# Kernel optimization log

Measured on AMD Instinct MI355X. Metric: run time of the kernel, lower is better.

## Reference

```python
import jax, jax.numpy as jnp
import numpy as np

D_MODEL = 1024
NUM_HEADS = 16
D_K = D_MODEL // NUM_HEADS
B, T = 2, 2048


def setup_inputs() -> dict:
    key = jax.random.key(0)
    ks = jax.random.split(key, 9)
    s = 1.0 / np.sqrt(D_MODEL)
    inp = {"x": jax.random.normal(ks[0], (B, T, D_MODEL), dtype=jnp.float32)}
    for i, name in enumerate(["q", "k", "v", "out"]):
        inp[f"W_{name}"] = jax.random.uniform(ks[1 + 2 * i], (D_MODEL, D_MODEL), jnp.float32, -s, s)
        inp[f"b_{name}"] = jax.random.uniform(ks[2 + 2 * i], (D_MODEL,), jnp.float32, -s, s)
    return inp


def reference(x, W_q, b_q, W_k, b_k, W_v, b_v, W_out, b_out):
    b, t, _ = x.shape
    # torch Linear: y = x @ W.T + b
    def proj(inp, W, bias):
        y = inp @ W.T + bias
        return y.reshape(b, -1, NUM_HEADS, D_K).transpose(0, 2, 1, 3)  # [B,H,T,d_k]

    Q = proj(x, W_q, b_q)
    K = proj(x, W_k, b_k)
    V = proj(x, W_v, b_v)
    scores = jnp.einsum("bhqd,bhkd->bhqk", Q, K) / jnp.sqrt(jnp.float32(D_K))
    attn = jax.nn.softmax(scores, axis=-1)
    ctx = jnp.einsum("bhqk,bhkd->bhqd", attn, V)
    ctx = ctx.transpose(0, 2, 1, 3).reshape(b, t, D_MODEL)
    return ctx @ W_out.T + b_out
```

## Files before the change

kernel.cpp:

```cpp
#include <hip/hip_runtime.h>
#include <hip/hip_bf16.h>

typedef __attribute__((ext_vector_type(8))) short short8;
typedef __attribute__((ext_vector_type(4))) float floatx4;

__device__ __forceinline__ unsigned short f2b(float f) {
  unsigned int v;
  __builtin_memcpy(&v, &f, 4);
  unsigned int r = (v + 0x7FFFu + ((v >> 16) & 1u)) >> 16;
  return (unsigned short)r;
}

__device__ __forceinline__ unsigned int f2b_pk(float a, float b) {
#if __has_builtin(__builtin_amdgcn_cvt_pk_bf16_f32)
  typedef __attribute__((ext_vector_type(2))) __bf16 bf16x2;
  bf16x2 r = __builtin_amdgcn_cvt_pk_bf16_f32(a, b);
  unsigned int u;
  __builtin_memcpy(&u, &r, 4);
  return u;
#else
  return ((unsigned int)f2b(b) << 16) | (unsigned int)f2b(a);
#endif
}

__device__ __forceinline__ float fast_exp2(float x) {
#if __has_builtin(__builtin_amdgcn_exp2f)
  return __builtin_amdgcn_exp2f(x);
#else
  return __builtin_exp2f(x);
#endif
}

__device__ __forceinline__ void async_copy16(const void* g, void* l) {
  __builtin_amdgcn_global_load_lds(
      (const __attribute__((address_space(1))) unsigned int*)g,
      (__attribute__((address_space(3))) unsigned int*)l, 16, 0, 0);
}

#define QSCALE 0.18033688011112042f

__global__ __launch_bounds__(256) void cvt_all_kernel(
    const float* __restrict__ x,
    const float* __restrict__ w0, const float* __restrict__ w1,
    const float* __restrict__ w2, const float* __restrict__ w3,
    unsigned short* __restrict__ xb,
    unsigned short* __restrict__ d0, unsigned short* __restrict__ d1,
    unsigned short* __restrict__ d2, unsigned short* __restrict__ d3)
{
  int gid = blockIdx.x * 256 + threadIdx.x;
  const float* src;
  unsigned short* dst;
  size_t off;
  if (gid < (1 << 20)) {
    src = x; dst = xb; off = gid;
  } else {
    int g = gid - (1 << 20);
    int w = g >> 18;
    off = g & 0x3FFFF;
    src = (w == 0) ? w0 : (w == 1) ? w1 : (w == 2) ? w2 : w3;
    dst = (w == 0) ? d0 : (w == 1) ? d1 : (w == 2) ? d2 : d3;
  }
  floatx4 v = *(const floatx4*)(src + off * 4);
  unsigned int lo = f2b_pk(v[0], v[1]), hi = f2b_pk(v[2], v[3]);
  unsigned long long r = ((unsigned long long)hi << 32) | lo;
  *(unsigned long long*)(dst + off * 4) = r;
}

__global__ __launch_bounds__(256) void gemm_qkv_kernel(
    const unsigned short* __restrict__ A,
    const unsigned short* __restrict__ W0, const unsigned short* __restrict__ W1,
    const unsigned short* __restrict__ W2,
    const float* __restrict__ bias0, const float* __restrict__ bias1,
    const float* __restrict__ bias2,
    unsigned short* __restrict__ Qo, unsigned short* __restrict__ Ko,
    unsigned short* __restrict__ VTo)
{
  const int z = blockIdx.z;
  const unsigned short* W  = (z == 0) ? W0 : (z == 1) ? W1 : W2;
  const float* bias        = (z == 0) ? bias0 : (z == 1) ? bias1 : bias2;

  __shared__ alignas(16) unsigned short sA[128 * 32];
  __shared__ alignas(16) unsigned short sB[128 * 32];

  const int tid  = threadIdx.x;
  const int lane = tid & 63;
  const int wave = tid >> 6;
  const int col  = lane & 15;
  const int quad = lane >> 4;
  const int wm   = (wave >> 1) * 64;
  const int wn   = (wave & 1) * 64;
  const int m0   = blockIdx.y * 128;
  const int n0   = blockIdx.x * 128;

  floatx4 acc[4][4];
#pragma unroll
  for (int i = 0; i < 4; ++i)
#pragma unroll
    for (int j = 0; j < 4; ++j) acc[i][j] = (floatx4){0.f, 0.f, 0.f, 0.f};

  for (int k0 = 0; k0 < 1024; k0 += 32) {
    __syncthreads();
#pragma unroll
    for (int i = 0; i < 2; ++i) {
      int c   = i * 256 + tid;
      int row = c >> 2;
      int ko  = (c & 3) * 8;
      async_copy16(A + (size_t)(m0 + row) * 1024 + k0 + ko, sA + c * 8);
      async_copy16(W + (size_t)(n0 + row) * 1024 + k0 + ko, sB + c * 8);
    }
    __syncthreads();
    short8 af[4], bf[4];
#pragma unroll
    for (int mi = 0; mi < 4; ++mi)
      af[mi] = *(const short8*)(sA + (wm + mi * 16 + col) * 32 + quad * 8);
#pragma unroll
    for (int ni = 0; ni < 4; ++ni)
      bf[ni] = *(const short8*)(sB + (wn + ni * 16 + col) * 32 + quad * 8);
#pragma unroll
    for (int mi = 0; mi < 4; ++mi)
#pragma unroll
      for (int ni = 0; ni < 4; ++ni)
        acc[mi][ni] = __builtin_amdgcn_mfma_f32_16x16x32_bf16(af[mi], bf[ni], acc[mi][ni], 0, 0, 0);
  }

#pragma unroll
  for (int ni = 0; ni < 4; ++ni) {
    int n = n0 + wn + ni * 16 + col;
    float bv = bias[n];
#pragma unroll
    for (int mi = 0; mi < 4; ++mi) {
      int mbase = m0 + wm + mi * 16 + quad * 4;
#pragma unroll
      for (int r = 0; r < 4; ++r) {
        int m = mbase + r;
        float val = acc[mi][ni][r] + bv;
        if (z == 0) {
          Qo[(size_t)m * 1024 + n] = f2b(val * QSCALE);
        } else if (z == 1) {
          Ko[(size_t)m * 1024 + n] = f2b(val);
        } else {
          int d = n & 63, h = n >> 6;
          int bb = m >> 11, t = m & 2047;
          VTo[(((size_t)bb * 16 + h) * 64 + d) * 2048 + t] = f2b(val);
        }
      }
    }
  }
}

__global__ __launch_bounds__(256) void gemm_out_kernel(
    const unsigned short* __restrict__ A, const unsigned short* __restrict__ W,
    const float* __restrict__ bias, float* __restrict__ DF)
{
  __shared__ alignas(16) unsigned short sA[128 * 32];
  __shared__ alignas(16) unsigned short sB[64 * 32];

  const int tid  = threadIdx.x;
  const int lane = tid & 63;
  const int wave = tid >> 6;
  const int col  = lane & 15;
  const int quad = lane >> 4;
  const int wm   = (wave >> 1) * 64;
  const int wn   = (wave & 1) * 32;
  const int m0   = blockIdx.y * 128;
  const int n0   = blockIdx.x * 64;

  floatx4 acc[4][2];
#pragma unroll
  for (int i = 0; i < 4; ++i)
#pragma unroll
    for (int j = 0; j < 2; ++j) acc[i][j] = (floatx4){0.f, 0.f, 0.f, 0.f};

  for (int k0 = 0; k0 < 1024; k0 += 32) {
    __syncthreads();
#pragma unroll
    for (int i = 0; i < 2; ++i) {
      int c   = i * 256 + tid;
      int row = c >> 2;
      int ko  = (c & 3) * 8;
      async_copy16(A + (size_t)(m0 + row) * 1024 + k0 + ko, sA + c * 8);
    }
    {
      int row = tid >> 2;
      int ko  = (tid & 3) * 8;
      async_copy16(W + (size_t)(n0 + row) * 1024 + k0 + ko, sB + tid * 8);
    }
    __syncthreads();
    short8 af[4], bf[2];
#pragma unroll
    for (int mi = 0; mi < 4; ++mi)
      af[mi] = *(const short8*)(sA + (wm + mi * 16 + col) * 32 + quad * 8);
#pragma unroll
    for (int ni = 0; ni < 2; ++ni)
      bf[ni] = *(const short8*)(sB + (wn + ni * 16 + col) * 32 + quad * 8);
#pragma unroll
    for (int mi = 0; mi < 4; ++mi)
#pragma unroll
      for (int ni = 0; ni < 2; ++ni)
        acc[mi][ni] = __builtin_amdgcn_mfma_f32_16x16x32_bf16(af[mi], bf[ni], acc[mi][ni], 0, 0, 0);
  }

#pragma unroll
  for (int ni = 0; ni < 2; ++ni) {
    int n = n0 + wn + ni * 16 + col;
    float bv = bias[n];
#pragma unroll
    for (int mi = 0; mi < 4; ++mi) {
      int mbase = m0 + wm + mi * 16 + quad * 4;
#pragma unroll
      for (int r = 0; r < 4; ++r)
        DF[(size_t)(mbase + r) * 1024 + n] = acc[mi][ni][r] + bv;
    }
  }
}

__global__ __launch_bounds__(256) void attention_kernel(
    const unsigned short* __restrict__ Q, const unsigned short* __restrict__ K,
    const unsigned short* __restrict__ VT, unsigned short* __restrict__ CTX)
{
  __shared__ alignas(16) unsigned short sQ[2 * 64 * 32];
  __shared__ alignas(16) unsigned short sK[2 * 64 * 32];
  __shared__ alignas(16) unsigned short sV[2 * 64 * 32];
  __shared__ alignas(16) unsigned short sP[4][16 * 72];

  const int bh = blockIdx.x;
  const int b = bh >> 4, h = bh & 15;
  const int q0 = blockIdx.y * 64;
  const int tid  = threadIdx.x;
  const int lane = tid & 63;
  const int wave = tid >> 6;
  const int col  = lane & 15;
  const int quad = lane >> 4;

#pragma unroll
  for (int i = 0; i < 2; ++i) {
    int r = tid >> 2;
    int ko = (tid & 3) * 8;
    async_copy16(Q + (size_t)(b * 2048 + q0 + r) * 1024 + h * 64 + i * 32 + ko,
                 sQ + (i * 256 + tid) * 8);
  }
  __syncthreads();
  short8 qf[2];
  qf[0] = *(const short8*)(sQ + (wave * 16 + col) * 32 + quad * 8);
  qf[1] = *(const short8*)(sQ + 2048 + (wave * 16 + col) * 32 + quad * 8);

  floatx4 Oacc[4];
#pragma unroll
  for (int f = 0; f < 4; ++f) Oacc[f] = (floatx4){0.f, 0.f, 0.f, 0.f};
  float lacc = 0.f;

  unsigned short* myP = &sP[wave][0];

  for (int kt = 0; kt < 2048; kt += 64) {
    __syncthreads();
#pragma unroll
    for (int i = 0; i < 2; ++i) {
      int r = tid >> 2;
      int ko = (tid & 3) * 8;
      async_copy16(K + (size_t)(b * 2048 + kt + r) * 1024 + h * 64 + i * 32 + ko,
                   sK + (i * 256 + tid) * 8);
      async_copy16(VT + ((size_t)bh * 64 + r) * 2048 + kt + i * 32 + ko,
                   sV + (i * 256 + tid) * 8);
    }
    __syncthreads();

    floatx4 ST[4];
#pragma unroll
    for (int f = 0; f < 4; ++f) {
      ST[f] = (floatx4){0.f, 0.f, 0.f, 0.f};
      short8 kf0 = *(const short8*)(sK + (f * 16 + col) * 32 + quad * 8);
      ST[f] = __builtin_amdgcn_mfma_f32_16x16x32_bf16(kf0, qf[0], ST[f], 0, 0, 0);
      short8 kf1 = *(const short8*)(sK + 2048 + (f * 16 + col) * 32 + quad * 8);
      ST[f] = __builtin_amdgcn_mfma_f32_16x16x32_bf16(kf1, qf[1], ST[f], 0, 0, 0);
    }

#pragma unroll
    for (int f = 0; f < 4; ++f) {
      float p0 = fast_exp2(ST[f][0]);
      float p1 = fast_exp2(ST[f][1]);
      float p2 = fast_exp2(ST[f][2]);
      float p3 = fast_exp2(ST[f][3]);
      lacc += (p0 + p1) + (p2 + p3);
      unsigned long long w =
          ((unsigned long long)f2b_pk(p2, p3) << 32) | f2b_pk(p0, p1);
      *(unsigned long long*)(myP + col * 72 + f * 16 + quad * 4) = w;
    }

    short8 pf0 = *(const short8*)(myP + col * 72 + quad * 8);
    short8 pf1 = *(const short8*)(myP + col * 72 + 32 + quad * 8);
#pragma unroll
    for (int f = 0; f < 4; ++f) {
      short8 vf0 = *(const short8*)(sV + (f * 16 + col) * 32 + quad * 8);
      Oacc[f] = __builtin_amdgcn_mfma_f32_16x16x32_bf16(pf0, vf0, Oacc[f], 0, 0, 0);
      short8 vf1 = *(const short8*)(sV + 2048 + (f * 16 + col) * 32 + quad * 8);
      Oacc[f] = __builtin_amdgcn_mfma_f32_16x16x32_bf16(pf1, vf1, Oacc[f], 0, 0, 0);
    }
  }

  lacc += __shfl_xor(lacc, 16, 64);
  lacc += __shfl_xor(lacc, 32, 64);
  float inv[4];
#pragma unroll
  for (int r = 0; r < 4; ++r) inv[r] = 1.f / __shfl(lacc, quad * 4 + r, 16);

#pragma unroll
  for (int f = 0; f < 4; ++f) {
#pragma unroll
    for (int r = 0; r < 4; ++r) {
      int q = q0 + wave * 16 + quad * 4 + r;
      int d = f * 16 + col;
      CTX[(size_t)(b * 2048 + q) * 1024 + h * 64 + d] = f2b(Oacc[f][r] * inv[r]);
    }
  }
}

extern "C" void kernel_launch(void* const* d_in, const int* in_sizes, int n_in,
                              void* d_out, int out_size, void* d_ws, size_t ws_size,
                              hipStream_t stream) {
  const float* x   = (const float*)d_in[0];
  const float* W_q = (const float*)d_in[1];
  const float* b_q = (const float*)d_in[2];
  const float* W_k = (const float*)d_in[3];
  const float* b_k = (const float*)d_in[4];
  const float* W_v = (const float*)d_in[5];
  const float* b_v = (const float*)d_in[6];
  const float* W_o = (const float*)d_in[7];
  const float* b_o = (const float*)d_in[8];
  float* out = (float*)d_out;

  const size_t NX = (size_t)4096 * 1024;
  const size_t NW = (size_t)1024 * 1024;

  unsigned short* p   = (unsigned short*)d_ws;
  unsigned short* xb  = p;  p += NX;
  unsigned short* Wqb = p;  p += NW;
  unsigned short* Wkb = p;  p += NW;
  unsigned short* Wvb = p;  p += NW;
  unsigned short* Wob = p;  p += NW;
  unsigned short* Q   = p;  p += NX;
  unsigned short* Kb  = p;  p += NX;
  unsigned short* VT  = p;  p += NX;
  unsigned short* CTX = p;  p += NX;

  dim3 blk(256);
  cvt_all_kernel<<<dim3(8192), blk, 0, stream>>>(
      x, W_q, W_k, W_v, W_o, xb, Wqb, Wkb, Wvb, Wob);
  gemm_qkv_kernel<<<dim3(8, 32, 3), blk, 0, stream>>>(
      xb, Wqb, Wkb, Wvb, b_q, b_k, b_v, Q, Kb, VT);
  attention_kernel<<<dim3(32, 32), blk, 0, stream>>>(Q, Kb, VT, CTX);
  gemm_out_kernel<<<dim3(16, 32), blk, 0, stream>>>(CTX, Wob, b_o, out);
}
```

Baseline: 215.8 us.

## Split attention keys across waves with double-buffered K and barrier-free main loop

Each wave now handles all 64 queries of the block but only its own quarter of each 128-key tile. Per-wave K is double-buffered and V prefetched with async copies and manual waitcnt, which removes the two block-wide barriers per key tile. Partial outputs and row sums from the four waves are reduced through shared memory at the end, and the normalized context is written with 16-byte stores. In exchange the kernel holds many more accumulator registers, serializes a four-step cross-wave reduction, and relies on hand-coded waitcnt values being correct.

After: 229.2 us. +6.2%, slower.

```diff
diff --git a/kernel.cpp b/kernel.cpp
--- a/kernel.cpp
+++ b/kernel.cpp
@@ -2,6 +2,7 @@
 #include <hip/hip_bf16.h>
 
 typedef __attribute__((ext_vector_type(8))) short short8;
+typedef __attribute__((ext_vector_type(4))) short short4v;
 typedef __attribute__((ext_vector_type(4))) float floatx4;
 
 __device__ __forceinline__ unsigned short f2b(float f) {
@@ -218,10 +219,10 @@
     const unsigned short* __restrict__ Q, const unsigned short* __restrict__ K,
     const unsigned short* __restrict__ VT, unsigned short* __restrict__ CTX)
 {
-  __shared__ alignas(16) unsigned short sQ[2 * 64 * 32];
-  __shared__ alignas(16) unsigned short sK[2 * 64 * 32];
-  __shared__ alignas(16) unsigned short sV[2 * 64 * 32];
-  __shared__ alignas(16) unsigned short sP[4][16 * 72];
+  __shared__ alignas(16) unsigned short sKb[16384];
+  __shared__ alignas(16) unsigned short sVb[8192];
+  __shared__ alignas(16) unsigned short sPb[9216];
+  __shared__ float sL[4][64];
 
   const int bh = blockIdx.x;
   const int b = bh >> 4, h = bh & 15;
@@ -231,85 +232,171 @@
   const int wave = tid >> 6;
   const int col  = lane & 15;
   const int quad = lane >> 4;
-
-#pragma unroll
-  for (int i = 0; i < 2; ++i) {
-    int r = tid >> 2;
-    int ko = (tid & 3) * 8;
-    async_copy16(Q + (size_t)(b * 2048 + q0 + r) * 1024 + h * 64 + i * 32 + ko,
-                 sQ + (i * 256 + tid) * 8);
-  }
+  const int l4   = lane >> 2;
+  const int lo4  = (lane & 3) * 8;
+
+  const unsigned short* Kg = K + (size_t)(b * 2048) * 1024 + h * 64;
+  const unsigned short* Vg = VT + (size_t)bh * 64 * 2048;
+
+#pragma unroll
+  for (int s = 0; s < 2; ++s)
+    async_copy16(Q + (size_t)(b * 2048 + q0 + wave * 16 + l4) * 1024 + h * 64 + s * 32 + lo4,
+                 sPb + s * 2048 + wave * 512 + lane * 8);
+  {
+    unsigned short* kd = sKb + wave * 2048;
+#pragma unroll
+    for (int s = 0; s < 2; ++s)
+#pragma unroll
+      for (int j = 0; j < 2; ++j)
+        async_copy16(Kg + (size_t)(wave * 32 + j * 16 + l4) * 1024 + s * 32 + lo4,
+                     kd + s * 1024 + j * 512 + lane * 8);
+    unsigned short* vd = sVb + wave * 2048;
+#pragma unroll
+    for (int i = 0; i < 4; ++i)
+      async_copy16(Vg + (size_t)(i * 16 + l4) * 2048 + wave * 32 + lo4,
+                   vd + i * 512 + lane * 8);
+  }
+  __builtin_amdgcn_s_waitcnt(0xF70);
   __syncthreads();
-  short8 qf[2];
-  qf[0] = *(const short8*)(sQ + (wave * 16 + col) * 32 + quad * 8);
-  qf[1] = *(const short8*)(sQ + 2048 + (wave * 16 + col) * 32 + quad * 8);
-
-  floatx4 Oacc[4];
-#pragma unroll
-  for (int f = 0; f < 4; ++f) Oacc[f] = (floatx4){0.f, 0.f, 0.f, 0.f};
-  float lacc = 0.f;
-
-  unsigned short* myP = &sP[wave][0];
-
-  for (int kt = 0; kt < 2048; kt += 64) {
+
+  short8 qf[4][2];
+#pragma unroll
+  for (int qc = 0; qc < 4; ++qc)
+#pragma unroll
+    for (int s = 0; s < 2; ++s)
+      qf[qc][s] = *(const short8*)(sPb + s * 2048 + (qc * 16 + col) * 32 + quad * 8);
+  __syncthreads();
+
+  floatx4 Oacc[4][4];
+#pragma unroll
+  for (int mq = 0; mq < 4; ++mq)
+#pragma unroll
+    for (int nd = 0; nd < 4; ++nd) Oacc[mq][nd] = (floatx4){0.f, 0.f, 0.f, 0.f};
+  float lacc[4] = {0.f, 0.f, 0.f, 0.f};
+  unsigned short* myP = sPb + wave * 2304;
+  unsigned short* vw  = sVb + wave * 2048;
+
+  for (int t = 0; t < 16; ++t) {
+    const int buf = t & 1;
+    unsigned short* kw = sKb + buf * 8192 + wave * 2048;
+    const int ktn = (t + 1) * 128;
+
+    if (t < 15) {
+      unsigned short* kd = sKb + (buf ^ 1) * 8192 + wave * 2048;
+#pragma unroll
+      for (int s = 0; s < 2; ++s)
+#pragma unroll
+        for (int j = 0; j < 2; ++j)
+          async_copy16(Kg + (size_t)(ktn + wave * 32 + j * 16 + l4) * 1024 + s * 32 + lo4,
+                       kd + s * 1024 + j * 512 + lane * 8);
+      __builtin_amdgcn_s_waitcnt(0xF78);
+    } else {
+      __builtin_amdgcn_s_waitcnt(0xF74);
+    }
+
+    floatx4 ST[2][4];
+#pragma unroll
+    for (int kr = 0; kr < 2; ++kr)
+#pragma unroll
+      for (int qc = 0; qc < 4; ++qc) ST[kr][qc] = (floatx4){0.f, 0.f, 0.f, 0.f};
+#pragma unroll
+    for (int s = 0; s < 2; ++s) {
+      short8 k0 = *(const short8*)(kw + s * 1024 + col * 32 + quad * 8);
+      short8 k1 = *(const short8*)(kw + s * 1024 + (16 + col) * 32 + quad * 8);
+#pragma unroll
+      for (int qc = 0; qc < 4; ++qc) {
+        ST[0][qc] = __builtin_amdgcn_mfma_f32_16x16x32_bf16(k0, qf[qc][s], ST[0][qc], 0, 0, 0);
+        ST[1][qc] = __builtin_amdgcn_mfma_f32_16x16x32_bf16(k1, qf[qc][s], ST[1][qc], 0, 0, 0);
+      }
+    }
+
+#pragma unroll
+    for (int kr = 0; kr < 2; ++kr)
+#pragma unroll
+      for (int qc = 0; qc < 4; ++qc) {
+        float p0 = fast_exp2(ST[kr][qc][0]);
+        float p1 = fast_exp2(ST[kr][qc][1]);
+        float p2 = fast_exp2(ST[kr][qc][2]);
+        float p3 = fast_exp2(ST[kr][qc][3]);
+        lacc[qc] += (p0 + p1) + (p2 + p3);
+        unsigned long long pw =
+            ((unsigned long long)f2b_pk(p2, p3) << 32) | f2b_pk(p0, p1);
+        *(unsigned long long*)(myP + (qc * 16 + col) * 36 + kr * 16 + quad * 4) = pw;
+      }
+
+    short8 pf[4];
+#pragma unroll
+    for (int mq = 0; mq < 4; ++mq) {
+      const unsigned short* pp = myP + (mq * 16 + col) * 36 + quad * 8;
+      short4v plo = *(const short4v*)pp;
+      short4v phi = *(const short4v*)(pp + 4);
+      pf[mq] = (short8){plo[0], plo[1], plo[2], plo[3], phi[0], phi[1], phi[2], phi[3]};
+    }
+
+    if (t < 15) __builtin_amdgcn_s_waitcnt(0xF74);
+    else        __builtin_amdgcn_s_waitcnt(0xF70);
+
+    short8 vf[4];
+#pragma unroll
+    for (int nd = 0; nd < 4; ++nd)
+      vf[nd] = *(const short8*)(vw + (nd * 16 + col) * 32 + quad * 8);
+    __builtin_amdgcn_s_waitcnt(0xC07F);
+
+    if (t < 15) {
+#pragma unroll
+      for (int i = 0; i < 4; ++i)
+        async_copy16(Vg + (size_t)(i * 16 + l4) * 2048 + ktn + wave * 32 + lo4,
+                     vw + i * 512 + lane * 8);
+    }
+
+#pragma unroll
+    for (int nd = 0; nd < 4; ++nd)
+#pragma unroll
+      for (int mq = 0; mq < 4; ++mq)
+        Oacc[mq][nd] = __builtin_amdgcn_mfma_f32_16x16x32_bf16(pf[mq], vf[nd], Oacc[mq][nd], 0, 0, 0);
+  }
+
+#pragma unroll
+  for (int qc = 0; qc < 4; ++qc) {
+    lacc[qc] += __shfl_xor(lacc[qc], 16, 64);
+    lacc[qc] += __shfl_xor(lacc[qc], 32, 64);
+  }
+  if (quad == 0) {
+#pragma unroll
+    for (int qc = 0; qc < 4; ++qc) sL[wave][qc * 16 + col] = lacc[qc];
+  }
+
+  float* sO = (float*)sKb;
+#pragma unroll 1
+  for (int ww = 0; ww < 4; ++ww) {
     __syncthreads();
-#pragma unroll
-    for (int i = 0; i < 2; ++i) {
-      int r = tid >> 2;
-      int ko = (tid & 3) * 8;
-      async_copy16(K + (size_t)(b * 2048 + kt + r) * 1024 + h * 64 + i * 32 + ko,
-                   sK + (i * 256 + tid) * 8);
-      async_copy16(VT + ((size_t)bh * 64 + r) * 2048 + kt + i * 32 + ko,
-                   sV + (i * 256 + tid) * 8);
-    }
-    __syncthreads();
-
-    floatx4 ST[4];
-#pragma unroll
-    for (int f = 0; f < 4; ++f) {
-      ST[f] = (floatx4){0.f, 0.f, 0.f, 0.f};
-      short8 kf0 = *(const short8*)(sK + (f * 16 + col) * 32 + quad * 8);
-      ST[f] = __builtin_amdgcn_mfma_f32_16x16x32_bf16(kf0, qf[0], ST[f], 0, 0, 0);
-      short8 kf1 = *(const short8*)(sK + 2048 + (f * 16 + col) * 32 + quad * 8);
-      ST[f] = __builtin_amdgcn_mfma_f32_16x16x32_bf16(kf1, qf[1], ST[f], 0, 0, 0);
-    }
-
-#pragma unroll
-    for (int f = 0; f < 4; ++f) {
-      float p0 = fast_exp2(ST[f][0]);
-      float p1 = fast_exp2(ST[f][1]);
-      float p2 = fast_exp2(ST[f][2]);
-      float p3 = fast_exp2(ST[f][3]);
-      lacc += (p0 + p1) + (p2 + p3);
-      unsigned long long w =
-          ((unsigned long long)f2b_pk(p2, p3) << 32) | f2b_pk(p0, p1);
-      *(unsigned long long*)(myP + col * 72 + f * 16 + quad * 4) = w;
-    }
-
-    short8 pf0 = *(const short8*)(myP + col * 72 + quad * 8);
-    short8 pf1 = *(const short8*)(myP + col * 72 + 32 + quad * 8);
-#pragma unroll
-    for (int f = 0; f < 4; ++f) {
-      short8 vf0 = *(const short8*)(sV + (f * 16 + col) * 32 + quad * 8);
-      Oacc[f] = __builtin_amdgcn_mfma_f32_16x16x32_bf16(pf0, vf0, Oacc[f], 0, 0, 0);
-      short8 vf1 = *(const short8*)(sV + 2048 + (f * 16 + col) * 32 + quad * 8);
-      Oacc[f] = __builtin_amdgcn_mfma_f32_16x16x32_bf16(pf1, vf1, Oacc[f], 0, 0, 0);
-    }
-  }
-
-  lacc += __shfl_xor(lacc, 16, 64);
-  lacc += __shfl_xor(lacc, 32, 64);
-  float inv[4];
-#pragma unroll
-  for (int r = 0; r < 4; ++r) inv[r] = 1.f / __shfl(lacc, quad * 4 + r, 16);
-
-#pragma unroll
-  for (int f = 0; f < 4; ++f) {
-#pragma unroll
-    for (int r = 0; r < 4; ++r) {
-      int q = q0 + wave * 16 + quad * 4 + r;
-      int d = f * 16 + col;
-      CTX[(size_t)(b * 2048 + q) * 1024 + h * 64 + d] = f2b(Oacc[f][r] * inv[r]);
+    if (wave == ww) {
+#pragma unroll
+      for (int mq = 0; mq < 4; ++mq)
+#pragma unroll
+        for (int nd = 0; nd < 4; ++nd)
+#pragma unroll
+          for (int r = 0; r < 4; ++r) {
+            int idx = (mq * 16 + quad * 4 + r) * 64 + nd * 16 + col;
+            if (ww == 0) sO[idx] = Oacc[mq][nd][r];
+            else         sO[idx] += Oacc[mq][nd][r];
+          }
+    }
+  }
+  __syncthreads();
+
+  {
+    int q = tid >> 2, c = tid & 3;
+    float l = sL[0][q] + sL[1][q] + sL[2][q] + sL[3][q];
+    float inv = 1.f / l;
+    const float* row = sO + q * 64 + c * 16;
+    unsigned short* dst = CTX + (size_t)(b * 2048 + q0 + q) * 1024 + h * 64 + c * 16;
+#pragma unroll
+    for (int hf = 0; hf < 2; ++hf) {
+      alignas(16) unsigned short ob[8];
+#pragma unroll
+      for (int j = 0; j < 8; ++j) ob[j] = f2b(row[hf * 8 + j] * inv);
+      *(short8*)(dst + hf * 8) = *(const short8*)ob;
     }
   }
 }
```
